# Kernel tuning notes

Measured on AMD Instinct MI355X. Metric: run time of the kernel, lower is better.

Reference implementation:

```python
import jax, jax.numpy as jnp
import numpy as np

HIDDEN = 2048
HEADS = 16
HEAD_DIM = HIDDEN // HEADS
TOP_K = 256
B, N = 1, 2048


def setup_inputs() -> dict:
    key = jax.random.key(0)
    ks = jax.random.split(key, 9)
    s = 0.02
    return {
        "hidden_states": jax.random.normal(ks[0], (B, N, HIDDEN), jnp.float32),
        "Wq": jax.random.normal(ks[1], (HIDDEN, HIDDEN), jnp.float32) * s,
        "bq": jnp.zeros((HIDDEN,), jnp.float32),
        "Wk": jax.random.normal(ks[2], (HIDDEN, HIDDEN), jnp.float32) * s,
        "bk": jnp.zeros((HIDDEN,), jnp.float32),
        "Wv": jax.random.normal(ks[3], (HIDDEN, HIDDEN), jnp.float32) * s,
        "bv": jnp.zeros((HIDDEN,), jnp.float32),
        "Wo": jax.random.normal(ks[4], (HIDDEN, HIDDEN), jnp.float32) * s,
        "bo": jnp.zeros((HIDDEN,), jnp.float32),
    }


def _split_heads(x):
    b, n, _ = x.shape
    return x.reshape(b, n, HEADS, HEAD_DIM).transpose(0, 2, 1, 3)  # b h n d


def reference(hidden_states, Wq, bq, Wk, bk, Wv, bv, Wo, bo):
    scale = 1.0 / jnp.sqrt(jnp.float32(HEAD_DIM))
    q = _split_heads(hidden_states @ Wq + bq)  # [b,h,n,d]
    k = _split_heads(hidden_states @ Wk + bk)
    v = _split_heads(hidden_states @ Wv + bv)

    # Sparse path (kv_seq_length > attention_window): dense QK^T used only to rank keys.
    scores = jnp.einsum("bhnd,bhmd->bhnm", q, k) * scale  # [b,h,n,n]
    importance = scores.mean(axis=2)  # [b,h,n] aggregate over queries
    _, idx = jax.lax.top_k(importance, TOP_K)  # [b,h,k]

    # gather selected K/V (torch.gather along seq dim)
    k_sel = jnp.take_along_axis(k, idx[..., None], axis=2)  # [b,h,k,d]
    v_sel = jnp.take_along_axis(v, idx[..., None], axis=2)

    w = jax.nn.softmax(jnp.einsum("bhnd,bhkd->bhnk", q, k_sel) * scale, axis=-1)
    out = jnp.einsum("bhnk,bhkd->bhnd", w, v_sel)  # [b,h,n,d]
    out = out.transpose(0, 2, 1, 3).reshape(hidden_states.shape[0], -1, HIDDEN)
    return out @ Wo + bo
```

## Files before the change

### kernel.cpp

```cpp
#include <hip/hip_runtime.h>


typedef __attribute__((ext_vector_type(8))) short bf16x8;
typedef __attribute__((ext_vector_type(4))) float f32x4;

__device__ __forceinline__ unsigned short f2bf(float x) {
    unsigned u = __float_as_uint(x);
    u += 0x7fffu + ((u >> 16) & 1u);
    return (unsigned short)(u >> 16);
}

__device__ __forceinline__ void load_lds16(const unsigned short* g, unsigned short* l) {
    __builtin_amdgcn_global_load_lds(
        (const __attribute__((address_space(1))) unsigned int*)g,
        (__attribute__((address_space(3))) unsigned int*)l,
        16, 0, 0);
}

struct Ptr4  { const float* p[4]; };

__global__ __launch_bounds__(256) void gemm_qkv(
    const unsigned short* __restrict__ HSb,
    const unsigned short* __restrict__ WT4,
    const float* __restrict__ bq,
    const float* __restrict__ bk,
    const float* __restrict__ bv,
    const int* __restrict__ idx,
    unsigned short* __restrict__ Qb,
    unsigned short* __restrict__ Ksel,
    unsigned short* __restrict__ VselT)
{
    __shared__ __align__(16) unsigned short As[4][128][32];
    __shared__ __align__(16) unsigned short Bs[4][128][32];

    const int tid  = threadIdx.x;
    const int lane = tid & 63;
    const int wave = tid >> 6;
    const int wm = wave >> 1, wn = wave & 1;
    const int lr = lane >> 2;
    const int lc = (lane & 3) * 8;

    const int bid = blockIdx.x;

    int kv, h = 0, bm, bn;
    const unsigned short* Bt;
    long ar0, ar1;
    if (bid < 64) {
        kv = 1 + (bid >> 5);
        const int t = bid & 31;
        h  = t >> 1;
        bm = (t & 1) * 128;
        bn = h * 128;
        Bt = WT4 + (long)kv * 4194304;
        ar0 = idx[h * 256 + bm + wave * 16 + lr];
        ar1 = idx[h * 256 + bm + wave * 16 + 64 + lr];
    } else {
        kv = 0;
        const int t = bid - 64;
        const int st = t >> 4, u = t & 15;
        bm = ((st >> 2) * 4 + (u >> 2)) * 128;
        bn = ((st & 3) * 4 + (u & 3)) * 128;
        Bt = WT4;
        ar0 = bm + wave * 16 + lr;
        ar1 = ar0 + 64;
    }

    const unsigned short* Arow0 = HSb + ar0 * 2048 + lc;
    const unsigned short* Arow1 = HSb + ar1 * 2048 + lc;
    const unsigned short* Brow0 = Bt + (long)(bn + wave * 16 + lr) * 2048 + lc;
    const unsigned short* Brow1 = Brow0 + 64 * 2048;

    f32x4 acc[4][4];
#pragma unroll
    for (int i = 0; i < 4; i++)
#pragma unroll
        for (int j = 0; j < 4; j++) acc[i][j] = f32x4{0.f, 0.f, 0.f, 0.f};

    auto stage = [&](int b, int step) {
        const int k0 = step * 32;
        load_lds16(Arow0 + k0, &As[b][wave * 16][0]);
        load_lds16(Brow0 + k0, &Bs[b][wave * 16][0]);
        load_lds16(Arow1 + k0, &As[b][wave * 16 + 64][0]);
        load_lds16(Brow1 + k0, &Bs[b][wave * 16 + 64][0]);
    };
    auto compute = [&](int b) {
        bf16x8 af[4], bf[4];
#pragma unroll
        for (int s = 0; s < 4; s++)
            af[s] = *(const bf16x8*)&As[b][wm * 64 + s * 16 + (lane & 15)][(lane >> 4) * 8];
#pragma unroll
        for (int t = 0; t < 4; t++)
            bf[t] = *(const bf16x8*)&Bs[b][wn * 64 + t * 16 + (lane & 15)][(lane >> 4) * 8];
#pragma unroll
        for (int s = 0; s < 4; s++)
#pragma unroll
            for (int t = 0; t < 4; t++)
                acc[s][t] = __builtin_amdgcn_mfma_f32_16x16x32_bf16(af[s], bf[t], acc[s][t], 0, 0, 0);
    };

    stage(0, 0);
    stage(1, 1);
    stage(2, 2);
#pragma unroll 4
    for (int t = 0; t < 61; ++t) {
        asm volatile("s_waitcnt vmcnt(8)" ::: "memory");
        __builtin_amdgcn_s_barrier();
        __builtin_amdgcn_sched_barrier(0);
        stage((t + 3) & 3, t + 3);
        __builtin_amdgcn_sched_barrier(0);
        compute(t & 3);
    }
    asm volatile("s_waitcnt vmcnt(8)" ::: "memory");
    __builtin_amdgcn_s_barrier();
    __builtin_amdgcn_sched_barrier(0);
    compute(1);
    asm volatile("s_waitcnt vmcnt(4)" ::: "memory");
    __builtin_amdgcn_s_barrier();
    __builtin_amdgcn_sched_barrier(0);
    compute(2);
    asm volatile("s_waitcnt vmcnt(0)" ::: "memory");
    __builtin_amdgcn_s_barrier();
    __builtin_amdgcn_sched_barrier(0);
    compute(3);

    if (kv == 0) {
#pragma unroll
        for (int s = 0; s < 4; s++) {
#pragma unroll
            for (int t = 0; t < 4; t++) {
                const int col  = bn + wn * 64 + t * 16 + (lane & 15);
                const int row0 = bm + wm * 64 + s * 16 + (lane >> 4) * 4;
                const float bb = bq[col];
#pragma unroll
                for (int r = 0; r < 4; r++)
                    Qb[(long)(row0 + r) * 2048 + col] = f2bf(acc[s][t][r] + bb);
            }
        }
    } else {
        const float* bp = (kv == 1) ? bk : bv;
#pragma unroll
        for (int s = 0; s < 4; s++) {
#pragma unroll
            for (int t = 0; t < 4; t++) {
                const int col = bn + wn * 64 + t * 16 + (lane & 15);
                const int dd  = col & 127;
                const float bb = bp[col];
                const int j0 = bm + wm * 64 + s * 16 + (lane >> 4) * 4;
#pragma unroll
                for (int r = 0; r < 4; r++) {
                    const int j = j0 + r;
                    const unsigned short h16 = f2bf(acc[s][t][r] + bb);
                    if (kv == 1) Ksel [h * 32768 + j * 128 + dd] = h16;
                    else         VselT[h * 32768 + dd * 256 + j] = h16;
                }
            }
        }
    }
}

__global__ __launch_bounds__(256) void gemm_o(
    const unsigned short* __restrict__ Att,
    const unsigned short* __restrict__ WoT,
    float* __restrict__ Opart)
{
    __shared__ __align__(16) unsigned short As[4][128][32];
    __shared__ __align__(16) unsigned short Bs[4][128][32];

    const int tid  = threadIdx.x;
    const int lane = tid & 63;
    const int wave = tid >> 6;
    const int wm = wave >> 1, wn = wave & 1;
    const int lr = lane >> 2;
    const int lc = (lane & 3) * 8;

    const int bm = blockIdx.y * 128;
    const int bn = blockIdx.x * 128;
    const int b  = blockIdx.z;

    const unsigned short* Arow0 = Att + b * 1024 + (long)(bm + wave * 16 + lr) * 2048 + lc;
    const unsigned short* Arow1 = Arow0 + 64 * 2048;
    const unsigned short* Brow0 = WoT + b * 1024 + (long)(bn + wave * 16 + lr) * 2048 + lc;
    const unsigned short* Brow1 = Brow0 + 64 * 2048;

    f32x4 acc[4][4];
#pragma unroll
    for (int i = 0; i < 4; i++)
#pragma unroll
        for (int j = 0; j < 4; j++) acc[i][j] = f32x4{0.f, 0.f, 0.f, 0.f};

    auto stage = [&](int bb, int step) {
        const int k0 = step * 32;
        load_lds16(Arow0 + k0, &As[bb][wave * 16][0]);
        load_lds16(Brow0 + k0, &Bs[bb][wave * 16][0]);
        load_lds16(Arow1 + k0, &As[bb][wave * 16 + 64][0]);
        load_lds16(Brow1 + k0, &Bs[bb][wave * 16 + 64][0]);
    };
    auto compute = [&](int bb) {
        bf16x8 af[4], bf[4];
#pragma unroll
        for (int s = 0; s < 4; s++)
            af[s] = *(const bf16x8*)&As[bb][wm * 64 + s * 16 + (lane & 15)][(lane >> 4) * 8];
#pragma unroll
        for (int t = 0; t < 4; t++)
            bf[t] = *(const bf16x8*)&Bs[bb][wn * 64 + t * 16 + (lane & 15)][(lane >> 4) * 8];
#pragma unroll
        for (int s = 0; s < 4; s++)
#pragma unroll
            for (int t = 0; t < 4; t++)
                acc[s][t] = __builtin_amdgcn_mfma_f32_16x16x32_bf16(af[s], bf[t], acc[s][t], 0, 0, 0);
    };

    stage(0, 0);
    stage(1, 1);
    stage(2, 2);
#pragma unroll 4
    for (int t = 0; t < 29; ++t) {
        asm volatile("s_waitcnt vmcnt(8)" ::: "memory");
        __builtin_amdgcn_s_barrier();
        __builtin_amdgcn_sched_barrier(0);
        stage((t + 3) & 3, t + 3);
        __builtin_amdgcn_sched_barrier(0);
        compute(t & 3);
    }
    asm volatile("s_waitcnt vmcnt(8)" ::: "memory");
    __builtin_amdgcn_s_barrier();
    __builtin_amdgcn_sched_barrier(0);
    compute(1);
    asm volatile("s_waitcnt vmcnt(4)" ::: "memory");
    __builtin_amdgcn_s_barrier();
    __builtin_amdgcn_sched_barrier(0);
    compute(2);
    asm volatile("s_waitcnt vmcnt(0)" ::: "memory");
    __builtin_amdgcn_s_barrier();
    __builtin_amdgcn_sched_barrier(0);
    compute(3);

#pragma unroll
    for (int s = 0; s < 4; s++) {
#pragma unroll
        for (int t = 0; t < 4; t++) {
            const int col  = bn + wn * 64 + t * 16 + (lane & 15);
            const int row0 = bm + wm * 64 + s * 16 + (lane >> 4) * 4;
#pragma unroll
            for (int r = 0; r < 4; r++)
                Opart[(long)b * 4194304 + (long)(row0 + r) * 2048 + col] = acc[s][t][r];
        }
    }
}

__global__ __launch_bounds__(256) void oreduce(const float* __restrict__ part,
                                               const float* __restrict__ bo,
                                               float* __restrict__ out) {
    const long i = ((long)blockIdx.x * 256 + threadIdx.x) * 4;
    float4 a = *(const float4*)(part + i);
    float4 b = *(const float4*)(part + 4194304 + i);
    const int col = (int)(i & 2047);
    float4 o;
    o.x = a.x + b.x + bo[col];
    o.y = a.y + b.y + bo[col + 1];
    o.z = a.z + b.z + bo[col + 2];
    o.w = a.w + b.w + bo[col + 3];
    *(float4*)(out + i) = o;
}

#define QS_OFF(c)  ((c) * 2048)
#define KS_OFF(c)  (4096 + (c) * 8192)
#define PS_OFF     0
#define VS_OFF(c)  (16896 + (c) * 4096)

__global__ __launch_bounds__(256, 2) void attn_kernel(
    const unsigned short* __restrict__ Qb,
    const unsigned short* __restrict__ Ksel,
    const unsigned short* __restrict__ VselT,
    unsigned short* __restrict__ Att)
{
    __shared__ __align__(16) unsigned short smem[25088];
    __shared__ float linv[64];

    const int tid  = threadIdx.x;
    const int lane = tid & 63;
    const int wave = tid >> 6;
    const int bm = blockIdx.x * 64;
    const int h  = blockIdx.y;
    const int lr = lane >> 2, lc = (lane & 3) * 8;

    const unsigned short* Kh = Ksel  + h * 32768;
    const unsigned short* Vh = VselT + h * 32768;

    f32x4 acc[16];
#pragma unroll
    for (int t = 0; t < 16; t++) acc[t] = f32x4{0.f, 0.f, 0.f, 0.f};

#pragma unroll
    for (int c2 = 0; c2 < 2; c2++) {
        __syncthreads();
#pragma unroll
        for (int c = 0; c < 2; c++) {
            const int k0 = c2 * 64 + c * 32;
            load_lds16(Qb + (long)(bm + wave * 16 + lr) * 2048 + h * 128 + k0 + lc,
                       &smem[QS_OFF(c) + wave * 512]);
#pragma unroll
            for (int q = 0; q < 4; q++)
                load_lds16(Kh + (wave * 64 + q * 16 + lr) * 128 + k0 + lc,
                           &smem[KS_OFF(c) + (wave * 64 + q * 16) * 32]);
        }
        __syncthreads();
#pragma unroll
        for (int kk = 0; kk < 2; kk++) {
            bf16x8 af = *(const bf16x8*)&smem[QS_OFF(kk) + (wave * 16 + (lane & 15)) * 32 + (lane >> 4) * 8];
#pragma unroll
            for (int t = 0; t < 16; t++) {
                bf16x8 bfv = *(const bf16x8*)&smem[KS_OFF(kk) + (t * 16 + (lane & 15)) * 32 + (lane >> 4) * 8];
                acc[t] = __builtin_amdgcn_mfma_f32_16x16x32_bf16(af, bfv, acc[t], 0, 0, 0);
            }
        }
    }
    __syncthreads();

    const float se = 0.08838834764831845f * 1.4426950408889634f;
#pragma unroll
    for (int r = 0; r < 4; r++) {
        float mx = -3.0e38f;
#pragma unroll
        for (int t = 0; t < 16; t++) mx = fmaxf(mx, acc[t][r]);
#pragma unroll
        for (int off = 1; off < 16; off <<= 1) mx = fmaxf(mx, __shfl_xor(mx, off));
        float sum = 0.f;
#pragma unroll
        for (int t = 0; t < 16; t++) {
            float p = exp2f((acc[t][r] - mx) * se);
            acc[t][r] = p;
            sum += p;
        }
#pragma unroll
        for (int off = 1; off < 16; off <<= 1) sum += __shfl_xor(sum, off);
        const int row = wave * 16 + (lane >> 4) * 4 + r;
#pragma unroll
        for (int t = 0; t < 16; t++)
            smem[PS_OFF + row * 264 + t * 16 + (lane & 15)] = f2bf(acc[t][r]);
        if ((lane & 15) == 0) linv[row] = 1.0f / sum;
    }

    const int wm2 = wave >> 1, wn2 = wave & 1;
    f32x4 acc2[2][4];
#pragma unroll
    for (int i = 0; i < 2; i++)
#pragma unroll
        for (int j = 0; j < 4; j++) acc2[i][j] = f32x4{0.f, 0.f, 0.f, 0.f};

#pragma unroll
    for (int c2 = 0; c2 < 4; c2++) {
#pragma unroll
        for (int c = 0; c < 2; c++) {
            const int j0 = c2 * 64 + c * 32;
#pragma unroll
            for (int q = 0; q < 2; q++)
                load_lds16(Vh + (wave * 32 + q * 16 + lr) * 256 + j0 + lc,
                           &smem[VS_OFF(c) + (wave * 32 + q * 16) * 32]);
        }
        __syncthreads();
#pragma unroll
        for (int c = 0; c < 2; c++) {
            const int j0 = c2 * 64 + c * 32;
            bf16x8 af2[2], bf2v[4];
#pragma unroll
            for (int s2 = 0; s2 < 2; s2++)
                af2[s2] = *(const bf16x8*)&smem[PS_OFF + (wm2 * 32 + s2 * 16 + (lane & 15)) * 264 + j0 + (lane >> 4) * 8];
#pragma unroll
            for (int t2 = 0; t2 < 4; t2++)
                bf2v[t2] = *(const bf16x8*)&smem[VS_OFF(c) + (wn2 * 64 + t2 * 16 + (lane & 15)) * 32 + (lane >> 4) * 8];
#pragma unroll
            for (int s2 = 0; s2 < 2; s2++)
#pragma unroll
                for (int t2 = 0; t2 < 4; t2++)
                    acc2[s2][t2] = __builtin_amdgcn_mfma_f32_16x16x32_bf16(af2[s2], bf2v[t2], acc2[s2][t2], 0, 0, 0);
        }
        __syncthreads();
    }

#pragma unroll
    for (int s2 = 0; s2 < 2; s2++) {
#pragma unroll
        for (int t2 = 0; t2 < 4; t2++) {
            const int d = wn2 * 64 + t2 * 16 + (lane & 15);
#pragma unroll
            for (int r = 0; r < 4; r++) {
                const int row = wm2 * 32 + s2 * 16 + (lane >> 4) * 4 + r;
                float v = acc2[s2][t2][r] * linv[row];
                Att[(long)(bm + row) * 2048 + h * 128 + d] = f2bf(v);
            }
        }
    }
}

__global__ __launch_bounds__(256) void prep_kernel(Ptr4 srcs, unsigned short* __restrict__ WT4,
                                                   const float* __restrict__ hs,
                                                   double* __restrict__ part) {
    const int b = blockIdx.x;
    const int tid = threadIdx.x;
    if (b < 4096) {
        __shared__ float tile[64][65];
        const int z = b >> 10, xy = b & 1023;
        const float* W = srcs.p[z];
        unsigned short* WT = WT4 + (long)z * 4194304;
        const int bx = (xy & 31) * 64;
        const int by = (xy >> 5) * 64;
        const int x = tid & 63, y = tid >> 6;
#pragma unroll
        for (int i = 0; i < 64; i += 4)
            tile[y + i][x] = W[(long)(by + y + i) * 2048 + bx + x];
        __syncthreads();
#pragma unroll
        for (int i = 0; i < 64; i += 4)
            WT[(long)(bx + y + i) * 2048 + by + x] = f2bf(tile[x][y + i]);
    } else {
        const int c = b - 4096;
        const int col = (c & 7) * 256 + tid;
        const int r0  = (c >> 3) * 32;
        double a = 0.0;
#pragma unroll 4
        for (int r = 0; r < 32; r++) a += (double)hs[(long)(r0 + r) * 2048 + col];
        part[(long)(c >> 3) * 2048 + col] = a;
    }
}

__global__ void fill_kernel(float* p, float v, long n) {
    long i = ((long)blockIdx.x * blockDim.x + threadIdx.x) * 4;
    if (i + 3 < n) { p[i] = v; p[i+1] = v; p[i+2] = v; p[i+3] = v; }
}

__global__ __launch_bounds__(256) void mean_qsum_part(const double* __restrict__ part,
                                                      const float* __restrict__ Wq,
                                                      double* __restrict__ partq) {
    __shared__ float hsb[32];
    const int j  = blockIdx.x * 256 + threadIdx.x;
    const int i0 = blockIdx.y * 32;
    if (threadIdx.x < 32) {
        double s = 0.0;
#pragma unroll 4
        for (int g = 0; g < 64; g++) s += part[(long)g * 2048 + i0 + threadIdx.x];
        hsb[threadIdx.x] = (float)(s * (1.0 / 2048.0));
    }
    __syncthreads();
    double a = 0.0;
#pragma unroll 4
    for (int r = 0; r < 32; r++)
        a += (double)hsb[r] * (double)Wq[(long)(i0 + r) * 2048 + j];
    partq[(long)blockIdx.y * 2048 + j] = a;
}

__global__ void qsum_fin(const double* __restrict__ partq, const float* __restrict__ bq,
                         float* __restrict__ qbar) {
    const int j = blockIdx.x * 64 + threadIdx.x;
    double s = (double)bq[j];
#pragma unroll 4
    for (int g = 0; g < 64; g++) s += partq[(long)g * 2048 + j];
    qbar[j] = (float)s;
}

__global__ __launch_bounds__(256) void u_kernel(const float* __restrict__ Wk,
                                                const float* __restrict__ qbar,
                                                float* __restrict__ U) {
    const int i = blockIdx.x, t = threadIdx.x;
#pragma unroll
    for (int r = 0; r < 2; r++) {
        const int e = r * 1024 + t * 4;
        float4 w = *(const float4*)(Wk + (long)i * 2048 + e);
        float4 q = *(const float4*)(qbar + e);
        float a = w.x * q.x + w.y * q.y + w.z * q.z + w.w * q.w;
#pragma unroll
        for (int off = 16; off; off >>= 1) a += __shfl_xor(a, off);
        if ((t & 31) == 0) U[(long)i * 16 + r * 8 + (t >> 5)] = a;
    }
}

__global__ __launch_bounds__(256) void cast_imp_kernel(const float* __restrict__ hs,
                                                       const float* __restrict__ U,
                                                       unsigned short* __restrict__ HSb,
                                                       float* __restrict__ imp) {
    __shared__ float row[2048];
    __shared__ float red[4][16];
    const int m = blockIdx.x, t = threadIdx.x;
    for (int i = t; i < 2048; i += 256) {
        float v = hs[(long)m * 2048 + i];
        row[i] = v;
        HSb[(long)m * 2048 + i] = f2bf(v);
    }
    __syncthreads();
    float p[16];
#pragma unroll
    for (int h = 0; h < 16; h++) p[h] = 0.f;
    for (int i = t * 8; i < t * 8 + 8; i++) {
        const float v = row[i];
        const float* u = U + i * 16;
#pragma unroll
        for (int h = 0; h < 16; h++) p[h] += v * u[h];
    }
#pragma unroll
    for (int off = 32; off; off >>= 1)
#pragma unroll
        for (int h = 0; h < 16; h++) p[h] += __shfl_down(p[h], off);
    if ((t & 63) == 0)
#pragma unroll
        for (int h = 0; h < 16; h++) red[t >> 6][h] = p[h];
    __syncthreads();
    if (t < 16)
        imp[(long)t * 2048 + m] = red[0][t] + red[1][t] + red[2][t] + red[3][t];
}

__global__ __launch_bounds__(64) void topk_idx(const float* __restrict__ imp,
                                               int* __restrict__ idx) {
    const int h = blockIdx.x;
    const int lane = threadIdx.x;
    unsigned u[32];
#pragma unroll
    for (int r = 0; r < 32; r++) {
        unsigned x = __float_as_uint(imp[(long)h * 2048 + r * 64 + lane]);
        u[r] = (x & 0x80000000u) ? ~x : (x | 0x80000000u);
    }
    unsigned cur = 0;
    for (int b = 31; b >= 0; b--) {
        const unsigned cand = cur | (1u << b);
        int tot = 0;
#pragma unroll
        for (int r = 0; r < 32; r++)
            tot += (int)__popcll(__ballot(u[r] >= cand));
        if (tot >= 256) cur = cand;
    }
    const unsigned long long below = (1ull << lane) - 1ull;
    int pos[32];
    int base = 0;
#pragma unroll
    for (int r = 0; r < 32; r++) {
        const bool q = u[r] > cur;
        const unsigned long long m = __ballot(q);
        pos[r] = q ? base + (int)__popcll(m & below) : -1;
        base += (int)__popcll(m);
    }
#pragma unroll
    for (int r = 0; r < 32; r++) {
        const bool q = (u[r] == cur);
        const unsigned long long m = __ballot(q);
        if (q) {
            const int p = base + (int)__popcll(m & below);
            pos[r] = (p < 256) ? p : -1;
        }
        base += (int)__popcll(m);
    }
#pragma unroll
    for (int r = 0; r < 32; r++)
        if (pos[r] >= 0) idx[h * 256 + pos[r]] = r * 64 + lane;
}

extern "C" void kernel_launch(void* const* d_in, const int* in_sizes, int n_in,
                              void* d_out, int out_size, void* d_ws, size_t ws_size,
                              hipStream_t stream)
{
    const float* hs = (const float*)d_in[0];
    const float* Wq = (const float*)d_in[1];
    const float* bq = (const float*)d_in[2];
    const float* Wk = (const float*)d_in[3];
    const float* bk = (const float*)d_in[4];
    const float* Wv = (const float*)d_in[5];
    const float* bv = (const float*)d_in[6];
    const float* Wo = (const float*)d_in[7];
    const float* bo = (const float*)d_in[8];

    char* ws = (char*)d_ws;
    size_t off = 0;
    auto alloc = [&](size_t b) -> void* {
        void* p = ws + off;
        off = (off + b + 255) & ~(size_t)255;
        return p;
    };
    unsigned short* HSb   = (unsigned short*)alloc(8388608);
    unsigned short* WT4   = (unsigned short*)alloc(4 * 8388608);
    unsigned short* Qb    = (unsigned short*)alloc(8388608);
    unsigned short* Att   = (unsigned short*)alloc(8388608);
    unsigned short* Ksel  = (unsigned short*)alloc(1048576);
    unsigned short* VselT = (unsigned short*)alloc(1048576);
    float* Opart = (float*)alloc(2 * 16777216);
    double* part  = (double*)alloc(1048576);
    double* partq = (double*)alloc(1048576);
    float* qbar  = (float*)alloc(8192);
    float* U     = (float*)alloc(131072);
    float* imp   = (float*)alloc(131072);
    int*   idx   = (int*)alloc(16384);

    if (off > ws_size) {
        fill_kernel<<<4096, 256, 0, stream>>>((float*)d_out, 12345.0f, (long)out_size);
        return;
    }

    unsigned short* WoT = WT4 + 3 * 4194304;

    prep_kernel<<<4608, 256, 0, stream>>>(Ptr4{{Wq, Wk, Wv, Wo}}, WT4, hs, part);

    mean_qsum_part<<<dim3(8, 64), 256, 0, stream>>>(part, Wq, partq);
    qsum_fin<<<32, 64, 0, stream>>>(partq, bq, qbar);
    u_kernel<<<2048, 256, 0, stream>>>(Wk, qbar, U);
    cast_imp_kernel<<<2048, 256, 0, stream>>>(hs, U, HSb, imp);

    topk_idx<<<16, 64, 0, stream>>>(imp, idx);

    gemm_qkv<<<320, 256, 0, stream>>>(HSb, WT4, bq, bk, bv, idx, Qb, Ksel, VselT);

    attn_kernel<<<dim3(32, 16), 256, 0, stream>>>(Qb, Ksel, VselT, Att);

    gemm_o<<<dim3(16, 16, 2), 256, 0, stream>>>(Att, WoT, Opart);

    oreduce<<<4096, 256, 0, stream>>>(Opart, bo, (float*)d_out);
}
```

Baseline: 310.7 us.

## Use 128x64 GEMM tiles, drop split-K output GEMM and reduction kernel

The QKV and output GEMMs move from 128x128 tiles to 128x64 tiles, doubling the block count (640 and 512) to fill more CUs. The output GEMM no longer splits K in two with an fp32 partial buffer. It now runs the full K loop and adds the bias directly, so the separate oreduce kernel and its 32MB partial write and read go away. The cost is lower arithmetic intensity per tile and more redundant A-tile loads across blocks.

```diff
diff --git a/kernel.cpp b/kernel.cpp
--- a/kernel.cpp
+++ b/kernel.cpp
@@ -31,7 +31,7 @@
     unsigned short* __restrict__ VselT)
 {
     __shared__ __align__(16) unsigned short As[4][128][32];
-    __shared__ __align__(16) unsigned short Bs[4][128][32];
+    __shared__ __align__(16) unsigned short Bs[4][64][32];
 
     const int tid  = threadIdx.x;
     const int lane = tid & 63;
@@ -45,21 +45,21 @@
     int kv, h = 0, bm, bn;
     const unsigned short* Bt;
     long ar0, ar1;
-    if (bid < 64) {
-        kv = 1 + (bid >> 5);
-        const int t = bid & 31;
-        h  = t >> 1;
-        bm = (t & 1) * 128;
-        bn = h * 128;
+    if (bid < 128) {
+        kv = 1 + (bid >> 6);
+        const int t = bid & 63;
+        h  = t >> 2;
+        bm = ((t >> 1) & 1) * 128;
+        bn = h * 128 + (t & 1) * 64;
         Bt = WT4 + (long)kv * 4194304;
         ar0 = idx[h * 256 + bm + wave * 16 + lr];
         ar1 = idx[h * 256 + bm + wave * 16 + 64 + lr];
     } else {
         kv = 0;
-        const int t = bid - 64;
-        const int st = t >> 4, u = t & 15;
-        bm = ((st >> 2) * 4 + (u >> 2)) * 128;
-        bn = ((st & 3) * 4 + (u & 3)) * 128;
+        const int t = bid - 128;
+        const int st = t >> 5, u = t & 31;
+        bm = ((st >> 2) * 4 + (u >> 3)) * 128;
+        bn = ((st & 3) * 8 + (u & 7)) * 64;
         Bt = WT4;
         ar0 = bm + wave * 16 + lr;
         ar1 = ar0 + 64;
@@ -68,33 +68,31 @@
     const unsigned short* Arow0 = HSb + ar0 * 2048 + lc;
     const unsigned short* Arow1 = HSb + ar1 * 2048 + lc;
     const unsigned short* Brow0 = Bt + (long)(bn + wave * 16 + lr) * 2048 + lc;
-    const unsigned short* Brow1 = Brow0 + 64 * 2048;
-
-    f32x4 acc[4][4];
+
+    f32x4 acc[4][2];
 #pragma unroll
     for (int i = 0; i < 4; i++)
 #pragma unroll
-        for (int j = 0; j < 4; j++) acc[i][j] = f32x4{0.f, 0.f, 0.f, 0.f};
+        for (int j = 0; j < 2; j++) acc[i][j] = f32x4{0.f, 0.f, 0.f, 0.f};
 
     auto stage = [&](int b, int step) {
         const int k0 = step * 32;
         load_lds16(Arow0 + k0, &As[b][wave * 16][0]);
+        load_lds16(Arow1 + k0, &As[b][wave * 16 + 64][0]);
         load_lds16(Brow0 + k0, &Bs[b][wave * 16][0]);
-        load_lds16(Arow1 + k0, &As[b][wave * 16 + 64][0]);
-        load_lds16(Brow1 + k0, &Bs[b][wave * 16 + 64][0]);
     };
     auto compute = [&](int b) {
-        bf16x8 af[4], bf[4];
+        bf16x8 af[4], bf[2];
 #pragma unroll
         for (int s = 0; s < 4; s++)
             af[s] = *(const bf16x8*)&As[b][wm * 64 + s * 16 + (lane & 15)][(lane >> 4) * 8];
 #pragma unroll
-        for (int t = 0; t < 4; t++)
-            bf[t] = *(const bf16x8*)&Bs[b][wn * 64 + t * 16 + (lane & 15)][(lane >> 4) * 8];
+        for (int t = 0; t < 2; t++)
+            bf[t] = *(const bf16x8*)&Bs[b][wn * 32 + t * 16 + (lane & 15)][(lane >> 4) * 8];
 #pragma unroll
         for (int s = 0; s < 4; s++)
 #pragma unroll
-            for (int t = 0; t < 4; t++)
+            for (int t = 0; t < 2; t++)
                 acc[s][t] = __builtin_amdgcn_mfma_f32_16x16x32_bf16(af[s], bf[t], acc[s][t], 0, 0, 0);
     };
 
@@ -103,18 +101,18 @@
     stage(2, 2);
 #pragma unroll 4
     for (int t = 0; t < 61; ++t) {
-        asm volatile("s_waitcnt vmcnt(8)" ::: "memory");
+        asm volatile("s_waitcnt vmcnt(6)" ::: "memory");
         __builtin_amdgcn_s_barrier();
         __builtin_amdgcn_sched_barrier(0);
         stage((t + 3) & 3, t + 3);
         __builtin_amdgcn_sched_barrier(0);
         compute(t & 3);
     }
-    asm volatile("s_waitcnt vmcnt(8)" ::: "memory");
+    asm volatile("s_waitcnt vmcnt(6)" ::: "memory");
     __builtin_amdgcn_s_barrier();
     __builtin_amdgcn_sched_barrier(0);
     compute(1);
-    asm volatile("s_waitcnt vmcnt(4)" ::: "memory");
+    asm volatile("s_waitcnt vmcnt(3)" ::: "memory");
     __builtin_amdgcn_s_barrier();
     __builtin_amdgcn_sched_barrier(0);
     compute(2);
@@ -127,8 +125,8 @@
 #pragma unroll
         for (int s = 0; s < 4; s++) {
 #pragma unroll
-            for (int t = 0; t < 4; t++) {
-                const int col  = bn + wn * 64 + t * 16 + (lane & 15);
+            for (int t = 0; t < 2; t++) {
+                const int col  = bn + wn * 32 + t * 16 + (lane & 15);
                 const int row0 = bm + wm * 64 + s * 16 + (lane >> 4) * 4;
                 const float bb = bq[col];
 #pragma unroll
@@ -141,8 +139,8 @@
 #pragma unroll
         for (int s = 0; s < 4; s++) {
 #pragma unroll
-            for (int t = 0; t < 4; t++) {
-                const int col = bn + wn * 64 + t * 16 + (lane & 15);
+            for (int t = 0; t < 2; t++) {
+                const int col = bn + wn * 32 + t * 16 + (lane & 15);
                 const int dd  = col & 127;
                 const float bb = bp[col];
                 const int j0 = bm + wm * 64 + s * 16 + (lane >> 4) * 4;
@@ -161,10 +159,11 @@
 __global__ __launch_bounds__(256) void gemm_o(
     const unsigned short* __restrict__ Att,
     const unsigned short* __restrict__ WoT,
-    float* __restrict__ Opart)
+    const float* __restrict__ bo,
+    float* __restrict__ out)
 {
     __shared__ __align__(16) unsigned short As[4][128][32];
-    __shared__ __align__(16) unsigned short Bs[4][128][32];
+    __shared__ __align__(16) unsigned short Bs[4][64][32];
 
     const int tid  = threadIdx.x;
     const int lane = tid & 63;
@@ -173,40 +172,39 @@
     const int lr = lane >> 2;
     const int lc = (lane & 3) * 8;
 
-    const int bm = blockIdx.y * 128;
-    const int bn = blockIdx.x * 128;
-    const int b  = blockIdx.z;
-
-    const unsigned short* Arow0 = Att + b * 1024 + (long)(bm + wave * 16 + lr) * 2048 + lc;
+    const int t0 = blockIdx.x;
+    const int st = t0 >> 5, u = t0 & 31;
+    const int bm = ((st >> 2) * 4 + (u >> 3)) * 128;
+    const int bn = ((st & 3) * 8 + (u & 7)) * 64;
+
+    const unsigned short* Arow0 = Att + (long)(bm + wave * 16 + lr) * 2048 + lc;
     const unsigned short* Arow1 = Arow0 + 64 * 2048;
-    const unsigned short* Brow0 = WoT + b * 1024 + (long)(bn + wave * 16 + lr) * 2048 + lc;
-    const unsigned short* Brow1 = Brow0 + 64 * 2048;
-
-    f32x4 acc[4][4];
+    const unsigned short* Brow0 = WoT + (long)(bn + wave * 16 + lr) * 2048 + lc;
+
+    f32x4 acc[4][2];
 #pragma unroll
     for (int i = 0; i < 4; i++)
 #pragma unroll
-        for (int j = 0; j < 4; j++) acc[i][j] = f32x4{0.f, 0.f, 0.f, 0.f};
-
-    auto stage = [&](int bb, int step) {
+        for (int j = 0; j < 2; j++) acc[i][j] = f32x4{0.f, 0.f, 0.f, 0.f};
+
+    auto stage = [&](int b, int step) {
         const int k0 = step * 32;
-        load_lds16(Arow0 + k0, &As[bb][wave * 16][0]);
-        load_lds16(Brow0 + k0, &Bs[bb][wave * 16][0]);
-        load_lds16(Arow1 + k0, &As[bb][wave * 16 + 64][0]);
-        load_lds16(Brow1 + k0, &Bs[bb][wave * 16 + 64][0]);
+        load_lds16(Arow0 + k0, &As[b][wave * 16][0]);
+        load_lds16(Arow1 + k0, &As[b][wave * 16 + 64][0]);
+        load_lds16(Brow0 + k0, &Bs[b][wave * 16][0]);
     };
-    auto compute = [&](int bb) {
-        bf16x8 af[4], bf[4];
+    auto compute = [&](int b) {
+        bf16x8 af[4], bf[2];
 #pragma unroll
         for (int s = 0; s < 4; s++)
-            af[s] = *(const bf16x8*)&As[bb][wm * 64 + s * 16 + (lane & 15)][(lane >> 4) * 8];
-#pragma unroll
-        for (int t = 0; t < 4; t++)
-            bf[t] = *(const bf16x8*)&Bs[bb][wn * 64 + t * 16 + (lane & 15)][(lane >> 4) * 8];
+            af[s] = *(const bf16x8*)&As[b][wm * 64 + s * 16 + (lane & 15)][(lane >> 4) * 8];
+#pragma unroll
+        for (int t = 0; t < 2; t++)
+            bf[t] = *(const bf16x8*)&Bs[b][wn * 32 + t * 16 + (lane & 15)][(lane >> 4) * 8];
 #pragma unroll
         for (int s = 0; s < 4; s++)
 #pragma unroll
-            for (int t = 0; t < 4; t++)
+            for (int t = 0; t < 2; t++)
                 acc[s][t] = __builtin_amdgcn_mfma_f32_16x16x32_bf16(af[s], bf[t], acc[s][t], 0, 0, 0);
     };
 
@@ -214,19 +212,19 @@
     stage(1, 1);
     stage(2, 2);
 #pragma unroll 4
-    for (int t = 0; t < 29; ++t) {
-        asm volatile("s_waitcnt vmcnt(8)" ::: "memory");
+    for (int t = 0; t < 61; ++t) {
+        asm volatile("s_waitcnt vmcnt(6)" ::: "memory");
         __builtin_amdgcn_s_barrier();
         __builtin_amdgcn_sched_barrier(0);
         stage((t + 3) & 3, t + 3);
         __builtin_amdgcn_sched_barrier(0);
         compute(t & 3);
     }
-    asm volatile("s_waitcnt vmcnt(8)" ::: "memory");
+    asm volatile("s_waitcnt vmcnt(6)" ::: "memory");
     __builtin_amdgcn_s_barrier();
     __builtin_amdgcn_sched_barrier(0);
     compute(1);
-    asm volatile("s_waitcnt vmcnt(4)" ::: "memory");
+    asm volatile("s_waitcnt vmcnt(3)" ::: "memory");
     __builtin_amdgcn_s_barrier();
     __builtin_amdgcn_sched_barrier(0);
     compute(2);
@@ -238,29 +236,15 @@
 #pragma unroll
     for (int s = 0; s < 4; s++) {
 #pragma unroll
-        for (int t = 0; t < 4; t++) {
-            const int col  = bn + wn * 64 + t * 16 + (lane & 15);
+        for (int t = 0; t < 2; t++) {
+            const int col  = bn + wn * 32 + t * 16 + (lane & 15);
             const int row0 = bm + wm * 64 + s * 16 + (lane >> 4) * 4;
+            const float bb = bo[col];
 #pragma unroll
             for (int r = 0; r < 4; r++)
-                Opart[(long)b * 4194304 + (long)(row0 + r) * 2048 + col] = acc[s][t][r];
-        }
-    }
-}
-
-__global__ __launch_bounds__(256) void oreduce(const float* __restrict__ part,
-                                               const float* __restrict__ bo,
-                                               float* __restrict__ out) {
-    const long i = ((long)blockIdx.x * 256 + threadIdx.x) * 4;
-    float4 a = *(const float4*)(part + i);
-    float4 b = *(const float4*)(part + 4194304 + i);
-    const int col = (int)(i & 2047);
-    float4 o;
-    o.x = a.x + b.x + bo[col];
-    o.y = a.y + b.y + bo[col + 1];
-    o.z = a.z + b.z + bo[col + 2];
-    o.w = a.w + b.w + bo[col + 3];
-    *(float4*)(out + i) = o;
+                out[(long)(row0 + r) * 2048 + col] = acc[s][t][r] + bb;
+        }
+    }
 }
 
 #define QS_OFF(c)  ((c) * 2048)
@@ -579,7 +563,6 @@
     unsigned short* Att   = (unsigned short*)alloc(8388608);
     unsigned short* Ksel  = (unsigned short*)alloc(1048576);
     unsigned short* VselT = (unsigned short*)alloc(1048576);
-    float* Opart = (float*)alloc(2 * 16777216);
     double* part  = (double*)alloc(1048576);
     double* partq = (double*)alloc(1048576);
     float* qbar  = (float*)alloc(8192);
@@ -603,11 +586,9 @@
 
     topk_idx<<<16, 64, 0, stream>>>(imp, idx);
 
-    gemm_qkv<<<320, 256, 0, stream>>>(HSb, WT4, bq, bk, bv, idx, Qb, Ksel, VselT);
+    gemm_qkv<<<640, 256, 0, stream>>>(HSb, WT4, bq, bk, bv, idx, Qb, Ksel, VselT);
 
     attn_kernel<<<dim3(32, 16), 256, 0, stream>>>(Qb, Ksel, VselT, Att);
 
-    gemm_o<<<dim3(16, 16, 2), 256, 0, stream>>>(Att, WoT, Opart);
-
-    oreduce<<<4096, 256, 0, stream>>>(Opart, bo, (float*)d_out);
-}
+    gemm_o<<<512, 256, 0, stream>>>(Att, WoT, bo, (float*)d_out);
+}
```

Result: no change. 306.6 us (-1.3%).
